# Optimization experiments

Measured on AMD Instinct MI355X. Metric: run time of the kernel, lower is better.

## Reference

```python
import jax, jax.numpy as jnp
import numpy as np

N, IN, OUT, T = 262144, 128, 128, 8

def setup_inputs() -> dict:
    key = jax.random.key(0)
    k1, k2, k3, k4 = jax.random.split(key, 4)
    x = jax.random.normal(k1, (N, IN), dtype=jnp.float32)
    x_type = jax.random.randint(k2, (N,), 0, T, dtype=jnp.int32)
    bound = 1.0 / np.sqrt(IN)
    # TypedLinear weight: [num_types, in_size, out_size]
    W = jax.random.uniform(k3, (T, IN, OUT), minval=-bound, maxval=bound, dtype=jnp.float32)
    b = jax.random.uniform(k4, (T, OUT), minval=-bound, maxval=bound, dtype=jnp.float32)
    return {"x": x, "x_type": x_type, "W": W, "b": b}

def reference(x, x_type, W, b):
    # Per-sample typed linear: out[n] = x[n] @ W[x_type[n]] + b[x_type[n]]
    # Grouped-GEMM formulation: loop over the small fixed set of types,
    # masking contributions, to avoid gathering a [N, IN, OUT] weight tensor.
    num_types = W.shape[0]
    out = jnp.zeros((x.shape[0], W.shape[2]), dtype=x.dtype)
    for t in range(num_types):
        mask = (x_type == t).astype(x.dtype)[:, None]  # [N,1]
        out = out + (x @ W[t]) * mask
    out = out + b[x_type]  # type-indexed bias gather
    return out
```

## Files before the change

### kernel.cpp

```cpp
#include <hip/hip_runtime.h>
#include <hip/hip_bf16.h>

#define N_ROWS 262144
#define IN_DIM 128
#define OUT_DIM 128
#define NTYPES 8
#define ROWS_PER_BLOCK 256
#define GROUP_M 32
#define MAX_GROUPS 16

typedef short bf16x8 __attribute__((ext_vector_type(8)));
typedef float f32x4 __attribute__((ext_vector_type(4)));

__device__ __forceinline__ unsigned short f2bf_rne(float f) {
    unsigned int u = __float_as_uint(f);
    u += 0x7fff + ((u >> 16) & 1);
    return (unsigned short)(u >> 16);
}

__global__ void __launch_bounds__(128) prep_w_kernel(const float* __restrict__ W,
                                                     unsigned short* __restrict__ Wb) {
    const int t = blockIdx.x >> 7;
    const int o = blockIdx.x & 127;
    const int i = threadIdx.x;
    Wb[(t * OUT_DIM + o) * IN_DIM + i] = f2bf_rne(W[(t * IN_DIM + i) * OUT_DIM + o]);
}

__device__ __forceinline__ bf16x8 cvt_8f32_to_bf16(f32x4 f0, f32x4 f1) {
    union { bf16x8 v; __hip_bfloat162 h[4]; } u;
    u.h[0] = __float22bfloat162_rn(make_float2(f0[0], f0[1]));
    u.h[1] = __float22bfloat162_rn(make_float2(f0[2], f0[3]));
    u.h[2] = __float22bfloat162_rn(make_float2(f1[0], f1[1]));
    u.h[3] = __float22bfloat162_rn(make_float2(f1[2], f1[3]));
    return u.v;
}

__global__ void __launch_bounds__(256, 4) typed_linear_kernel(
        const float* __restrict__ x, const int* __restrict__ xt,
        const unsigned short* __restrict__ Wb, const float* __restrict__ bias,
        float* __restrict__ out) {
    __shared__ int s_cnt[NTYPES];
    __shared__ int s_cursor[NTYPES];
    __shared__ unsigned short s_list[ROWS_PER_BLOCK];
    __shared__ unsigned char s_gtype[MAX_GROUPS];
    __shared__ short s_gstart[MAX_GROUPS];
    __shared__ unsigned char s_gcnt[MAX_GROUPS];
    __shared__ int s_ngroups;
    __shared__ float s_bias[NTYPES * OUT_DIM];

    const int tid = threadIdx.x;
    const int row0 = blockIdx.x * ROWS_PER_BLOCK;

    if (tid < NTYPES) s_cnt[tid] = 0;
    __syncthreads();
    const int my_t = xt[row0 + tid];
    atomicAdd(&s_cnt[my_t], 1);
    reinterpret_cast<float4*>(s_bias)[tid] = reinterpret_cast<const float4*>(bias)[tid];
    __syncthreads();
    if (tid == 0) {
        int acc = 0, g = 0;
        for (int i = 0; i < NTYPES; ++i) {
            int c = s_cnt[i];
            s_cursor[i] = acc;
            for (int s = 0; s < c; s += GROUP_M) {
                s_gtype[g] = (unsigned char)i;
                s_gstart[g] = (short)(acc + s);
                s_gcnt[g] = (unsigned char)((c - s) < GROUP_M ? (c - s) : GROUP_M);
                ++g;
            }
            acc += c;
        }
        s_ngroups = g;
    }
    __syncthreads();
    {
        int pos = atomicAdd(&s_cursor[my_t], 1);
        s_list[pos] = (unsigned short)tid;
    }
    __syncthreads();

    const int wave = tid >> 6;
    const int lane = tid & 63;
    const int m = lane & 15;
    const int q = lane >> 4;
    const int ngroups = s_ngroups;

    for (int g = wave; g < ngroups; g += 4) {
        const int t  = s_gtype[g];
        const int gs = s_gstart[g];
        const int gc = s_gcnt[g];
        const bool two = (gc > 16);

        const int mm0 = (m < gc) ? m : (gc - 1);
        const float* ap0 = x + (size_t)(row0 + s_list[gs + mm0]) * IN_DIM + q * 8;

        bf16x8 afrag[2][4];
        #pragma unroll
        for (int kc = 0; kc < 4; ++kc) {
            const f32x4 f0 = __builtin_nontemporal_load(
                reinterpret_cast<const f32x4*>(ap0 + kc * 32));
            const f32x4 f1 = __builtin_nontemporal_load(
                reinterpret_cast<const f32x4*>(ap0 + kc * 32 + 4));
            afrag[0][kc] = cvt_8f32_to_bf16(f0, f1);
        }
        if (two) {
            const int r1 = 16 + m;
            const int mm1 = (r1 < gc) ? r1 : (gc - 1);
            const float* ap1 = x + (size_t)(row0 + s_list[gs + mm1]) * IN_DIM + q * 8;
            #pragma unroll
            for (int kc = 0; kc < 4; ++kc) {
                const f32x4 f0 = __builtin_nontemporal_load(
                    reinterpret_cast<const f32x4*>(ap1 + kc * 32));
                const f32x4 f1 = __builtin_nontemporal_load(
                    reinterpret_cast<const f32x4*>(ap1 + kc * 32 + 4));
                afrag[1][kc] = cvt_8f32_to_bf16(f0, f1);
            }
        }

        int orow0[4], orow1[4];
        #pragma unroll
        for (int r = 0; r < 4; ++r) {
            const int mr0 = q * 4 + r;
            orow0[r] = (mr0 < gc) ? (row0 + s_list[gs + mr0]) : -1;
            const int mr1 = 16 + q * 4 + r;
            orow1[r] = (mr1 < gc) ? (row0 + s_list[gs + mr1]) : -1;
        }

        const unsigned short* wt = Wb + t * (IN_DIM * OUT_DIM);
        const float* sb = s_bias + t * OUT_DIM;

        if (two) {
            #pragma unroll
            for (int nt = 0; nt < 8; ++nt) {
                const unsigned short* wcol = wt + (nt * 16 + m) * IN_DIM + q * 8;
                bf16x8 bfr[4];
                #pragma unroll
                for (int kc = 0; kc < 4; ++kc)
                    bfr[kc] = *reinterpret_cast<const bf16x8*>(wcol + kc * 32);
                f32x4 acc0 = {0.f, 0.f, 0.f, 0.f};
                f32x4 acc1 = {0.f, 0.f, 0.f, 0.f};
                #pragma unroll
                for (int kc = 0; kc < 4; ++kc) {
                    acc0 = __builtin_amdgcn_mfma_f32_16x16x32_bf16(afrag[0][kc], bfr[kc], acc0, 0, 0, 0);
                    acc1 = __builtin_amdgcn_mfma_f32_16x16x32_bf16(afrag[1][kc], bfr[kc], acc1, 0, 0, 0);
                }
                const float bv = sb[nt * 16 + m];
                #pragma unroll
                for (int r = 0; r < 4; ++r) {
                    if (orow0[r] >= 0)
                        __builtin_nontemporal_store(acc0[r] + bv,
                            &out[(size_t)orow0[r] * OUT_DIM + nt * 16 + m]);
                    if (orow1[r] >= 0)
                        __builtin_nontemporal_store(acc1[r] + bv,
                            &out[(size_t)orow1[r] * OUT_DIM + nt * 16 + m]);
                }
            }
        } else {
            #pragma unroll
            for (int nt = 0; nt < 8; ++nt) {
                const unsigned short* wcol = wt + (nt * 16 + m) * IN_DIM + q * 8;
                bf16x8 bfr[4];
                #pragma unroll
                for (int kc = 0; kc < 4; ++kc)
                    bfr[kc] = *reinterpret_cast<const bf16x8*>(wcol + kc * 32);
                f32x4 acc0 = {0.f, 0.f, 0.f, 0.f};
                #pragma unroll
                for (int kc = 0; kc < 4; ++kc)
                    acc0 = __builtin_amdgcn_mfma_f32_16x16x32_bf16(afrag[0][kc], bfr[kc], acc0, 0, 0, 0);
                const float bv = sb[nt * 16 + m];
                #pragma unroll
                for (int r = 0; r < 4; ++r) {
                    if (orow0[r] >= 0)
                        __builtin_nontemporal_store(acc0[r] + bv,
                            &out[(size_t)orow0[r] * OUT_DIM + nt * 16 + m]);
                }
            }
        }
    }
}

extern "C" void kernel_launch(void* const* d_in, const int* in_sizes, int n_in,
                              void* d_out, int out_size, void* d_ws, size_t ws_size,
                              hipStream_t stream) {
    const float* x  = (const float*)d_in[0];
    const int* xt   = (const int*)d_in[1];
    const float* W  = (const float*)d_in[2];
    const float* b  = (const float*)d_in[3];
    float* out      = (float*)d_out;
    unsigned short* Wb = (unsigned short*)d_ws;

    prep_w_kernel<<<NTYPES * OUT_DIM, 128, 0, stream>>>(W, Wb);
    typed_linear_kernel<<<N_ROWS / ROWS_PER_BLOCK, 256, 0, stream>>>(x, xt, Wb, b, out);
}
```

Baseline: 287.7 us.

## Stage MFMA outputs in LDS and write full output rows with float4 stores

```diff
diff --git a/kernel.cpp b/kernel.cpp
--- a/kernel.cpp
+++ b/kernel.cpp
@@ -6,8 +6,9 @@
 #define OUT_DIM 128
 #define NTYPES 8
 #define ROWS_PER_BLOCK 256
-#define GROUP_M 32
-#define MAX_GROUPS 16
+#define GROUP_M 16
+#define MAX_GROUPS 32
+#define ROW_PAD 132
 
 typedef short bf16x8 __attribute__((ext_vector_type(8)));
 typedef float f32x4 __attribute__((ext_vector_type(4)));
@@ -39,6 +40,7 @@
         const float* __restrict__ x, const int* __restrict__ xt,
         const unsigned short* __restrict__ Wb, const float* __restrict__ bias,
         float* __restrict__ out) {
+    __shared__ float s_out[4][GROUP_M * ROW_PAD];
     __shared__ int s_cnt[NTYPES];
     __shared__ int s_cursor[NTYPES];
     __shared__ unsigned short s_list[ROWS_PER_BLOCK];
@@ -84,96 +86,58 @@
     const int m = lane & 15;
     const int q = lane >> 4;
     const int ngroups = s_ngroups;
+    float* sow = s_out[wave];
 
     for (int g = wave; g < ngroups; g += 4) {
         const int t  = s_gtype[g];
         const int gs = s_gstart[g];
         const int gc = s_gcnt[g];
-        const bool two = (gc > 16);
 
         const int mm0 = (m < gc) ? m : (gc - 1);
         const float* ap0 = x + (size_t)(row0 + s_list[gs + mm0]) * IN_DIM + q * 8;
-
-        bf16x8 afrag[2][4];
+        bf16x8 afrag[4];
         #pragma unroll
         for (int kc = 0; kc < 4; ++kc) {
-            const f32x4 f0 = __builtin_nontemporal_load(
-                reinterpret_cast<const f32x4*>(ap0 + kc * 32));
-            const f32x4 f1 = __builtin_nontemporal_load(
-                reinterpret_cast<const f32x4*>(ap0 + kc * 32 + 4));
-            afrag[0][kc] = cvt_8f32_to_bf16(f0, f1);
-        }
-        if (two) {
-            const int r1 = 16 + m;
-            const int mm1 = (r1 < gc) ? r1 : (gc - 1);
-            const float* ap1 = x + (size_t)(row0 + s_list[gs + mm1]) * IN_DIM + q * 8;
-            #pragma unroll
-            for (int kc = 0; kc < 4; ++kc) {
-                const f32x4 f0 = __builtin_nontemporal_load(
-                    reinterpret_cast<const f32x4*>(ap1 + kc * 32));
-                const f32x4 f1 = __builtin_nontemporal_load(
-                    reinterpret_cast<const f32x4*>(ap1 + kc * 32 + 4));
-                afrag[1][kc] = cvt_8f32_to_bf16(f0, f1);
-            }
-        }
-
-        int orow0[4], orow1[4];
-        #pragma unroll
-        for (int r = 0; r < 4; ++r) {
-            const int mr0 = q * 4 + r;
-            orow0[r] = (mr0 < gc) ? (row0 + s_list[gs + mr0]) : -1;
-            const int mr1 = 16 + q * 4 + r;
-            orow1[r] = (mr1 < gc) ? (row0 + s_list[gs + mr1]) : -1;
+            const f32x4 f0 = *reinterpret_cast<const f32x4*>(ap0 + kc * 32);
+            const f32x4 f1 = *reinterpret_cast<const f32x4*>(ap0 + kc * 32 + 4);
+            afrag[kc] = cvt_8f32_to_bf16(f0, f1);
         }
 
         const unsigned short* wt = Wb + t * (IN_DIM * OUT_DIM);
         const float* sb = s_bias + t * OUT_DIM;
 
-        if (two) {
+        f32x4 acc[8];
+        #pragma unroll
+        for (int nt = 0; nt < 8; ++nt) {
+            const unsigned short* wcol = wt + (nt * 16 + m) * IN_DIM + q * 8;
+            bf16x8 bfr[4];
             #pragma unroll
-            for (int nt = 0; nt < 8; ++nt) {
-                const unsigned short* wcol = wt + (nt * 16 + m) * IN_DIM + q * 8;
-                bf16x8 bfr[4];
-                #pragma unroll
-                for (int kc = 0; kc < 4; ++kc)
-                    bfr[kc] = *reinterpret_cast<const bf16x8*>(wcol + kc * 32);
-                f32x4 acc0 = {0.f, 0.f, 0.f, 0.f};
-                f32x4 acc1 = {0.f, 0.f, 0.f, 0.f};
-                #pragma unroll
-                for (int kc = 0; kc < 4; ++kc) {
-                    acc0 = __builtin_amdgcn_mfma_f32_16x16x32_bf16(afrag[0][kc], bfr[kc], acc0, 0, 0, 0);
-                    acc1 = __builtin_amdgcn_mfma_f32_16x16x32_bf16(afrag[1][kc], bfr[kc], acc1, 0, 0, 0);
-                }
-                const float bv = sb[nt * 16 + m];
-                #pragma unroll
-                for (int r = 0; r < 4; ++r) {
-                    if (orow0[r] >= 0)
-                        __builtin_nontemporal_store(acc0[r] + bv,
-                            &out[(size_t)orow0[r] * OUT_DIM + nt * 16 + m]);
-                    if (orow1[r] >= 0)
-                        __builtin_nontemporal_store(acc1[r] + bv,
-                            &out[(size_t)orow1[r] * OUT_DIM + nt * 16 + m]);
-                }
-            }
-        } else {
+            for (int kc = 0; kc < 4; ++kc)
+                bfr[kc] = *reinterpret_cast<const bf16x8*>(wcol + kc * 32);
+            f32x4 a = {0.f, 0.f, 0.f, 0.f};
             #pragma unroll
-            for (int nt = 0; nt < 8; ++nt) {
-                const unsigned short* wcol = wt + (nt * 16 + m) * IN_DIM + q * 8;
-                bf16x8 bfr[4];
-                #pragma unroll
-                for (int kc = 0; kc < 4; ++kc)
-                    bfr[kc] = *reinterpret_cast<const bf16x8*>(wcol + kc * 32);
-                f32x4 acc0 = {0.f, 0.f, 0.f, 0.f};
-                #pragma unroll
-                for (int kc = 0; kc < 4; ++kc)
-                    acc0 = __builtin_amdgcn_mfma_f32_16x16x32_bf16(afrag[0][kc], bfr[kc], acc0, 0, 0, 0);
-                const float bv = sb[nt * 16 + m];
-                #pragma unroll
-                for (int r = 0; r < 4; ++r) {
-                    if (orow0[r] >= 0)
-                        __builtin_nontemporal_store(acc0[r] + bv,
-                            &out[(size_t)orow0[r] * OUT_DIM + nt * 16 + m]);
-                }
+            for (int kc = 0; kc < 4; ++kc)
+                a = __builtin_amdgcn_mfma_f32_16x16x32_bf16(afrag[kc], bfr[kc], a, 0, 0, 0);
+            acc[nt] = a;
+        }
+
+        #pragma unroll
+        for (int nt = 0; nt < 8; ++nt) {
+            const float bv = sb[nt * 16 + m];
+            #pragma unroll
+            for (int r = 0; r < 4; ++r)
+                sow[(q * 4 + r) * ROW_PAD + nt * 16 + m] = acc[nt][r] + bv;
+        }
+
+        const int half = lane >> 5;
+        const int c4 = (lane & 31) * 4;
+        #pragma unroll
+        for (int j = 0; j < 8; ++j) {
+            const int rr = j * 2 + half;
+            if (rr < gc) {
+                const int orow = row0 + s_list[gs + rr];
+                const f32x4 v = *reinterpret_cast<const f32x4*>(&sow[rr * ROW_PAD + c4]);
+                *reinterpret_cast<f32x4*>(&out[(size_t)orow * OUT_DIM + c4]) = v;
             }
         }
     }
```

Result: slower. 315.6 us (+9.7%).
